# Optimization experiments

Hardware: AMD Instinct MI355X
Metric: run time of the kernel (lower is better)

## Reference

```python
import math
import jax, jax.numpy as jnp
import numpy as np
from jax import lax

B, S, D = 2, 1024, 768
H, E, DH = 12, 8, 64          # n_head, num_experts, head dim
KA = 1                        # top-k experts per head (attention)
KF = 2                        # top-k experts per token (FFN)
DFF = 2048
EMA_DECAY = 0.99
CAP_FACTOR = 1.25
NEG_INF = -1e9


def setup_inputs() -> dict:
    key = jax.random.key(0)
    ks = jax.random.split(key, 16)
    sc = 0.02
    x = jax.random.normal(ks[0], (B, S, D), jnp.float32)
    causal = jnp.tril(jnp.ones((S, S), jnp.float32))
    mask = jnp.where(causal > 0, 0.0, NEG_INF).astype(jnp.float32)
    return {
        "x": x,
        "mask": mask,
        "W_q": jax.random.normal(ks[1], (D, D), jnp.float32) * sc,
        "W_k": jax.random.normal(ks[2], (D, D), jnp.float32) * sc,
        "W_v": jax.random.normal(ks[3], (H, E, DH, DH), jnp.float32) * sc,
        "W_o": jax.random.normal(ks[4], (H, E, DH, DH), jnp.float32) * sc,
        "W_router": jax.random.normal(ks[5], (D, H * E), jnp.float32) * sc,
        "g1": jnp.ones((D,), jnp.float32),
        "b1": jnp.zeros((D,), jnp.float32),
        "g2": jnp.ones((D,), jnp.float32),
        "b2": jnp.zeros((D,), jnp.float32),
        "gate_ff": jax.random.normal(ks[6], (D, E), jnp.float32) * sc,
        "W1": jax.random.normal(ks[7], (E, D, DFF), jnp.float32) * sc,
        "W2": jax.random.normal(ks[8], (E, DFF, D), jnp.float32) * sc,
    }


def layer_norm(x, g, b, eps=1e-5):
    m = jnp.mean(x, -1, keepdims=True)
    v = jnp.var(x, -1, keepdims=True)
    return (x - m) * lax.rsqrt(v + eps) * g + b


def head_switch_attention(x, mask, W_q, W_k, W_v, W_o, W_router):
    b, s, d = x.shape
    q = (x @ W_q).reshape(b, s, H, DH)
    k = (x @ W_k).reshape(b, s, H, DH)
    scores = jnp.einsum("bshd,bthd->bhst", q, k) / math.sqrt(DH) + mask
    p_attn = jax.nn.softmax(scores, axis=-1)          # (B,H,S,S)
    gate_logits = (x @ W_router).reshape(b, s, H, E)
    topk_scores, topk_idx = lax.top_k(gate_logits, KA)  # (B,S,H,KA)
    probs = jax.nn.softmax(topk_scores, axis=-1)
    x_h = x.reshape(b, s, H, DH)
    # value projections for all experts (small d_h x d_h GEMMs)
    v_all = jnp.einsum("bshd,hedf->bshef", x_h, W_v)
    y = jnp.zeros_like(x_h)
    hard_counts = jnp.zeros((H, E), jnp.float32)
    for slot in range(KA):
        oh = jax.nn.one_hot(topk_idx[..., slot], E, dtype=x.dtype)  # (B,S,H,E)
        v_sel = jnp.einsum("bshef,bshe->bshf", v_all, oh)
        # faithful to original einsum 'bhst,hbsd->hbtd' (sums over s)
        attn_out = jnp.einsum("bhst,bshf->bthf", p_attn, v_sel)
        o_all = jnp.einsum("bthf,hefg->btheg", attn_out, W_o)
        o_sel = jnp.einsum("btheg,bthe->bthg", o_all, oh)
        y = y + o_sel * probs[..., slot][..., None]
        hard_counts = hard_counts + lax.stop_gradient(oh).sum((0, 1))
    y = y.reshape(b, s, d)
    # EMA buffers start at zero -> ema = (1-decay)*hard/denom
    ema = hard_counts / (b * s * KA) * (1.0 - EMA_DECAY)
    p_lb = ema / (ema.sum() + 1e-9)
    aux = (p_lb * p_lb).sum() * E * H
    return y, aux


def moe_ffn(x, gate_ff, W1, W2):
    b, s, d = x.shape
    gate_logits = x @ gate_ff                      # (B,S,E), eval: no noise
    topk_scores, topk_idx = lax.top_k(gate_logits, KF)
    probs = jax.nn.softmax(topk_scores, axis=-1)   # (B,S,KF)
    capacity = math.ceil(CAP_FACTOR * (b * s) / E)
    flat_idx = topk_idx.reshape(-1)                # (B*S*KF,)
    oh_flat = jax.nn.one_hot(flat_idx, E, dtype=jnp.float32)
    tokens_so_far = jnp.cumsum(oh_flat, axis=0)
    keep = jnp.take_along_axis(tokens_so_far <= capacity, flat_idx[:, None], axis=1)[:, 0]
    probs = probs * keep.reshape(b, s, KF).astype(probs.dtype)
    probs = probs / (probs.sum(-1, keepdims=True) + 1e-9)
    oh = jax.nn.one_hot(topk_idx, E, dtype=probs.dtype)   # (B,S,KF,E)
    w = (probs[..., None] * oh).sum(2).reshape(b * s, E)  # combined weight per (token, expert)
    xf = x.reshape(b * s, d)
    yf = jnp.zeros_like(xf)
    for e in range(E):
        # scaling applied BEFORE ReLU, matching original x_sel = x * weight
        xe = xf * w[:, e:e + 1]
        yf = yf + jnp.maximum(xe @ W1[e], 0.0) @ W2[e]
    token_ctr = ((probs > 0)[..., None].astype(jnp.float32) * oh).sum((0, 1, 2))
    imp_ctr = (probs[..., None] * oh).sum((0, 1, 2))
    aux = ((token_ctr / token_ctr.sum()) * (imp_ctr / imp_ctr.sum())).sum() * E
    return yf.reshape(b, s, d), aux


def reference(x, mask, W_q, W_k, W_v, W_o, W_router, g1, b1, g2, b2, gate_ff, W1, W2):
    # pre-norm transformer block: x + Attn(LN(x)); x + MoEFFN(LN(x))
    a, aux1 = head_switch_attention(layer_norm(x, g1, b1), mask, W_q, W_k, W_v, W_o, W_router)
    x1 = x + a  # dropout is identity in eval
    f, aux2 = moe_ffn(layer_norm(x1, g2, b2), gate_ff, W1, W2)
    return x1 + f, aux1 + aux2
```

## Files before the change

### kernel.cpp

```cpp
#include <hip/hip_runtime.h>
#include <hip/hip_bf16.h>
#include <cstdint>

typedef __hip_bfloat16 bf16;
typedef __attribute__((ext_vector_type(8))) __bf16 bfrag;
typedef __attribute__((ext_vector_type(4))) float f32x4;

#define B_    2
#define S_    1024
#define D_    768
#define H_    12
#define E_    8
#define DH_   64
#define DFF_  2048
#define CAP_  320
#define CAPP_ 384
#define NTOK  (B_*S_)
#define NTH   (NTOK*H_)
#define QKLD  1536
#define NHE   (H_*E_)

__device__ __forceinline__ void stage16(const bf16* g, bf16* ldsLane){
#if __has_builtin(__builtin_amdgcn_global_load_lds)
  __builtin_amdgcn_global_load_lds((const __attribute__((address_space(1))) unsigned int*)g,
                                   (__attribute__((address_space(3))) unsigned int*)ldsLane, 16, 0, 0);
#else
  *(bfrag*)ldsLane = *(const bfrag*)g;
#endif
}

__global__ __launch_bounds__(256)
void transp_all(const float* __restrict__ Wq, const float* __restrict__ Wk,
                const float* __restrict__ Wr, const float* __restrict__ W1,
                const float* __restrict__ W2,
                bf16* __restrict__ WcatB, float* __restrict__ WrT,
                bf16* __restrict__ WT1, bf16* __restrict__ WT2)
{
  __shared__ float t[64][65];
  int bid = blockIdx.x;
  int tid = threadIdx.x;
  if (bid < 6432){
    const float* src; int N, K, bx, by; bf16* dst;
    if (bid < 144){      src = Wq; N = 768;  K = 768;  bx = bid % 12; by = bid / 12; dst = WcatB; }
    else if (bid < 288){ int r = bid - 144;  src = Wk; N = 768;  K = 768;  bx = r % 12; by = r / 12; dst = WcatB + (long)768*768; }
    else if (bid < 3360){int r = bid - 288;  int e = r / 384; r -= e*384;
                         src = W1 + (long)e*768*2048; N = 2048; K = 768;  bx = r % 32; by = r / 32; dst = WT1 + (long)e*2048*768; }
    else {               int r = bid - 3360; int e = r / 384; r -= e*384;
                         src = W2 + (long)e*2048*768; N = 768;  K = 2048; bx = r % 12; by = r / 12; dst = WT2 + (long)e*768*2048; }
    int n0 = bx*64, k0 = by*64;
    int chunk = tid & 15, rbase = tid >> 4;
#pragma unroll
    for (int rr=0; rr<4; rr++){
      int row = rr*16 + rbase;
      float4 v = *(const float4*)(src + (long)(k0+row)*N + n0 + chunk*4);
      t[row][chunk*4+0] = v.x; t[row][chunk*4+1] = v.y;
      t[row][chunk*4+2] = v.z; t[row][chunk*4+3] = v.w;
    }
    __syncthreads();
#pragma unroll
    for (int rr=0; rr<4; rr++){
      int n = rr*16 + rbase;
      union { ushort4 u; bf16 h[4]; } o;
      o.h[0] = __float2bfloat16(t[chunk*4+0][n]);
      o.h[1] = __float2bfloat16(t[chunk*4+1][n]);
      o.h[2] = __float2bfloat16(t[chunk*4+2][n]);
      o.h[3] = __float2bfloat16(t[chunk*4+3][n]);
      *(ushort4*)(dst + (long)(n0+n)*K + k0 + chunk*4) = o.u;
    }
  } else {
    int r = bid - 6432;
    int n0 = (r % 3)*32, k0 = (r / 3)*64;
    int chunk = tid & 7, row2 = tid >> 3;
#pragma unroll
    for (int rr=0; rr<2; rr++){
      int row = rr*32 + row2;
      float4 v = *(const float4*)(Wr + (long)(k0+row)*96 + n0 + chunk*4);
      t[row][chunk*4+0] = v.x; t[row][chunk*4+1] = v.y;
      t[row][chunk*4+2] = v.z; t[row][chunk*4+3] = v.w;
    }
    __syncthreads();
    int chunkw = tid & 15, nb = tid >> 4;
#pragma unroll
    for (int rr=0; rr<2; rr++){
      int n = rr*16 + nb;
      float4 o;
      o.x = t[chunkw*4+0][n]; o.y = t[chunkw*4+1][n];
      o.z = t[chunkw*4+2][n]; o.w = t[chunkw*4+3][n];
      *(float4*)(WrT + (long)(n0+n)*768 + k0 + chunkw*4) = o;
    }
  }
}

__global__ __launch_bounds__(256)
void gemm_bn64(const bf16* __restrict__ A, const bf16* __restrict__ Bt,
               void* __restrict__ C, void* __restrict__ C2,
               int M, int N, int K, long sA, long sB, long sC, int relu, int outBf, int kSplit)
{
  int nwg = gridDim.x*gridDim.y*gridDim.z;
  int bid = blockIdx.x + gridDim.x*(blockIdx.y + gridDim.y*blockIdx.z);
  int nid = (bid & 7)*(nwg >> 3) + (bid >> 3);
  int bx = nid % gridDim.x;
  int t1 = nid / gridDim.x;
  int by = t1 % gridDim.y;
  int bz = t1 / gridDim.y;
  int e  = bz / kSplit, kc = bz - e*kSplit;
  A  += (long)e*sA;
  Bt += (long)e*sB;
  int kLen = K / kSplit, kBase = kc*kLen;
  int m0 = by*128, n0 = bx*64;
  __shared__ bf16 As[2][128*32];
  __shared__ bf16 Bs[2][64*32];
  int tid = threadIdx.x;
  int w = tid >> 6, lane = tid & 63;
  int quad = lane >> 4, l16 = lane & 15;
  int wm = w*32;
  f32x4 acc[2][4] = {};
  int srow = (lane >> 2);
  int gsw  = ((lane & 3) ^ (srow & 3))*8;
  const bf16* aBase = A + (long)m0*K;
  const bf16* bBase = Bt + (long)n0*K;
  int xr = (l16 & 3);
  int nIt = kLen >> 5;
  {
    int k0 = kBase;
#pragma unroll
    for (int j=0;j<2;j++){
      int c = w*2 + j, row = c*16 + srow;
      stage16(aBase + (long)row*K + k0 + gsw, As[0] + c*512 + lane*8);
    }
    int rowb = w*16 + srow;
    stage16(bBase + (long)rowb*K + k0 + gsw, Bs[0] + w*512 + lane*8);
  }
  int cur = 0;
  for (int it=0; it<nIt; ++it){
    __syncthreads();
    if (it+1 < nIt){
      int k0 = kBase + (it+1)*32;
      int nb = cur^1;
#pragma unroll
      for (int j=0;j<2;j++){
        int c = w*2 + j, row = c*16 + srow;
        stage16(aBase + (long)row*K + k0 + gsw, As[nb] + c*512 + lane*8);
      }
      int rowb = w*16 + srow;
      stage16(bBase + (long)rowb*K + k0 + gsw, Bs[nb] + w*512 + lane*8);
    }
    const bf16* Ac = As[cur];
    const bf16* Bc = Bs[cur];
    bfrag af[2], bfv[4];
#pragma unroll
    for (int t=0;t<2;t++) af[t]  = *(const bfrag*)(Ac + (wm + t*16 + l16)*32 + ((quad ^ xr)*8));
#pragma unroll
    for (int t=0;t<4;t++) bfv[t] = *(const bfrag*)(Bc + (t*16 + l16)*32 + ((quad ^ xr)*8));
#pragma unroll
    for (int ti=0;ti<2;ti++)
#pragma unroll
      for (int tj=0;tj<4;tj++)
        acc[ti][tj] = __builtin_amdgcn_mfma_f32_16x16x32_bf16(af[ti], bfv[tj], acc[ti][tj], 0, 0, 0);
    cur ^= 1;
  }
  long zoff = (long)e*sC;
  void* Cp = kc ? C2 : C;
  if (outBf){
    bf16* Cb = (bf16*)Cp + zoff;
#pragma unroll
    for (int ti=0;ti<2;ti++)
#pragma unroll
      for (int tj=0;tj<4;tj++)
#pragma unroll
        for (int r=0;r<4;r++){
          int row = m0 + wm + ti*16 + quad*4 + r;
          int col = n0 + tj*16 + l16;
          float v = acc[ti][tj][r];
          if (relu) v = fmaxf(v, 0.f);
          Cb[(long)row*N + col] = __float2bfloat16(v);
        }
  } else {
    float* Cf = (float*)Cp + zoff;
#pragma unroll
    for (int ti=0;ti<2;ti++)
#pragma unroll
      for (int tj=0;tj<4;tj++)
#pragma unroll
        for (int r=0;r<4;r++){
          int row = m0 + wm + ti*16 + quad*4 + r;
          int col = n0 + tj*16 + l16;
          float v = acc[ti][tj][r];
          if (relu) v = fmaxf(v, 0.f);
          Cf[(long)row*N + col] = v;
        }
  }
}

__global__ __launch_bounds__(256)
void ln_kernel(const float* __restrict__ src, const float* __restrict__ g, const float* __restrict__ bb,
               float* __restrict__ dstF, bf16* __restrict__ dstB,
               const float* __restrict__ gateW, float* __restrict__ glog2)
{
  int row = blockIdx.x, tid = threadIdx.x;
  __shared__ float red[256];
  __shared__ float gsum[4][E_];
  float v[3];
#pragma unroll
  for (int j=0;j<3;j++) v[j] = src[(long)row*D_ + tid + j*256];
  float s = v[0]+v[1]+v[2];
  red[tid]=s; __syncthreads();
  for (int o=128;o>0;o>>=1){ if(tid<o) red[tid]+=red[tid+o]; __syncthreads(); }
  float mean = red[0]*(1.0f/D_);
  __syncthreads();
  float sq = 0.f;
#pragma unroll
  for (int j=0;j<3;j++){ float d=v[j]-mean; sq += d*d; }
  red[tid]=sq; __syncthreads();
  for (int o=128;o>0;o>>=1){ if(tid<o) red[tid]+=red[tid+o]; __syncthreads(); }
  float rstd = rsqrtf(red[0]*(1.0f/D_) + 1e-5f);
  float ov[3];
#pragma unroll
  for (int j=0;j<3;j++){
    int d = tid + j*256;
    float o = (v[j]-mean)*rstd*g[d] + bb[d];
    ov[j] = o;
    dstF[(long)row*D_+d] = o;
    if (dstB) dstB[(long)row*D_+d] = __float2bfloat16(o);
  }
  if (gateW){
    float gp[E_] = {};
#pragma unroll
    for (int j=0;j<3;j++){
      int d = tid + j*256;
      const float* gw = gateW + (long)d*E_;
#pragma unroll
      for (int e=0;e<E_;e++) gp[e] += ov[j]*gw[e];
    }
#pragma unroll
    for (int off=1; off<64; off<<=1)
#pragma unroll
      for (int e=0;e<E_;e++) gp[e] += __shfl_xor(gp[e], off);
    if ((tid & 63) == 0)
#pragma unroll
      for (int e=0;e<E_;e++) gsum[tid>>6][e] = gp[e];
    __syncthreads();
    if (tid < E_)
      glog2[(long)row*E_ + tid] = gsum[0][tid]+gsum[1][tid]+gsum[2][tid]+gsum[3][tid];
  }
}

#define RTOK 4
__global__ __launch_bounds__(768)
void router_argmax(const float* __restrict__ ln1, const float* __restrict__ WrT,
                   int* __restrict__ eidx, int* __restrict__ gHist,
                   int* __restrict__ hCnt, int* __restrict__ hList)
{
  int tok0 = blockIdx.x*RTOK;
  int tid = threadIdx.x;
  int col = tid >> 3, seg = tid & 7;
  __shared__ float xrow[RTOK][D_];
  __shared__ float logits[RTOK][96];
  for (int i=tid; i<RTOK*D_; i+=768){
    int t = i / D_, dpos = i - t*D_;
    xrow[t][dpos] = ln1[(long)(tok0+t)*D_ + dpos];
  }
  __syncthreads();
  const float* wrow = WrT + (long)col*D_;
  float acc[RTOK] = {};
#pragma unroll
  for (int j=0;j<24;j++){
    int dbase = j*32 + seg*4;
    float4 w = *(const float4*)(wrow + dbase);
#pragma unroll
    for (int t=0;t<RTOK;t++){
      float4 xv = *(const float4*)(&xrow[t][dbase]);
      acc[t] += xv.x*w.x + xv.y*w.y + xv.z*w.z + xv.w*w.w;
    }
  }
#pragma unroll
  for (int off=1; off<8; off<<=1)
#pragma unroll
    for (int t=0;t<RTOK;t++) acc[t] += __shfl_xor(acc[t], off);
  if (seg == 0)
#pragma unroll
    for (int t=0;t<RTOK;t++) logits[t][col] = acc[t];
  __syncthreads();
  if (tid < RTOK*H_){
    int t = tid / H_, h = tid % H_;
    const float* p = &logits[t][h*8];
    float best = p[0]; int bi = 0;
#pragma unroll
    for (int e=1;e<8;e++){ float v=p[e]; if (v > best){ best=v; bi=e; } }
    int tok = tok0 + t;
    eidx[tok*H_ + h] = bi;
    atomicAdd(&gHist[h*E_ + bi], 1);
    int he = h*E_ + bi;
    int pos = atomicAdd(&hCnt[he], 1);
    hList[he*NTOK + pos] = tok;
  }
}

__global__ __launch_bounds__(256)
void vsel_b(const float* __restrict__ ln1, const float* __restrict__ Wv,
            const int* __restrict__ hCnt, const int* __restrict__ hList,
            bf16* __restrict__ vT)
{
  int he = blockIdx.x;
  int h = he >> 3;
  __shared__ float Ws[DH_*DH_];
  __shared__ float xsh[4][DH_];
  int tid = threadIdx.x;
  const float* W = Wv + (long)he*DH_*DH_;
  for (int i=tid; i<DH_*DH_; i+=256) Ws[i] = W[i];
  int cnt = hCnt[he];
  __syncthreads();
  int w = tid >> 6, lane = tid & 63;
  const int* lst = hList + (long)he*NTOK;
  for (int i = blockIdx.y*4 + w; i < cnt; i += 32){
    int tok = lst[i];
    int b = tok >> 10, s = tok & 1023;
    xsh[w][lane] = ln1[(long)tok*D_ + h*DH_ + lane];
    float acc = 0.f;
#pragma unroll 8
    for (int d=0; d<DH_; d++) acc += xsh[w][d]*Ws[d*DH_ + lane];
    vT[((long)(b*H_+h)*DH_ + lane)*S_ + s] = __float2bfloat16(acc);
  }
}

__global__ __launch_bounds__(256)
void attn_stats_mfma(const bf16* __restrict__ qkB, float* __restrict__ gM, float* __restrict__ gL)
{
  int h = blockIdx.y, b = blockIdx.z;
  int tid = threadIdx.x;
  int w = tid >> 6, lane = tid & 63;
  int quad = lane >> 4, l16 = lane & 15;
  int x7 = l16 & 7;
  __shared__ bf16 ldsQ[64*64];
  __shared__ bf16 ldsK[2][64*64];
  const bf16* kbase = qkB + ((long)(b*S_))*QKLD + 768 + h*DH_;
  for (int half=0; half<2; half++){
    int s0 = (half ? (S_/64 - 1 - blockIdx.x) : blockIdx.x)*64;
    __syncthreads();
    const bf16* qbase = qkB + ((long)(b*S_ + s0))*QKLD + h*DH_;
#pragma unroll
    for (int j=0;j<2;j++){
      int c = j*256 + tid;
      int row = c >> 3;
      int gs = ((c & 7) ^ (row & 7))*8;
      stage16(qbase + (long)row*QKLD + gs, ldsQ + c*8);
      stage16(kbase + (long)row*QKLD + gs, ldsK[0] + c*8);
    }
    float m_ln[4] = {-1e30f,-1e30f,-1e30f,-1e30f};
    float l_ln[4] = {0.f,0.f,0.f,0.f};
    int ttEnd = s0 >> 6;
    int cur = 0;
    for (int tt=0; tt<=ttEnd; tt++){
      __syncthreads();
      if (tt < ttEnd){
#pragma unroll
        for (int j=0;j<2;j++){
          int c = j*256 + tid;
          int row = c >> 3;
          int gs = ((c & 7) ^ (row & 7))*8;
          stage16(kbase + (long)((tt+1)*64 + row)*QKLD + gs, ldsK[cur^1] + c*8);
        }
      }
      const bf16* Kc = ldsK[cur];
      bfrag af0 = *(const bfrag*)(ldsQ + (w*16 + l16)*64 + ((quad     ^ x7)*8));
      bfrag af1 = *(const bfrag*)(ldsQ + (w*16 + l16)*64 + (((quad+4) ^ x7)*8));
      f32x4 cfr[4];
#pragma unroll
      for (int j=0;j<4;j++){
        bfrag b0 = *(const bfrag*)(Kc + (j*16 + l16)*64 + ((quad     ^ x7)*8));
        bfrag b1 = *(const bfrag*)(Kc + (j*16 + l16)*64 + (((quad+4) ^ x7)*8));
        f32x4 z = {};
        z = __builtin_amdgcn_mfma_f32_16x16x32_bf16(af0, b0, z, 0,0,0);
        z = __builtin_amdgcn_mfma_f32_16x16x32_bf16(af1, b1, z, 0,0,0);
        cfr[j] = z;
      }
#pragma unroll
      for (int r=0;r<4;r++){
        int s_g = s0 + w*16 + quad*4 + r;
        float v0 = (tt*64      + l16 <= s_g) ? cfr[0][r]*0.125f : -1e30f;
        float v1 = (tt*64 + 16 + l16 <= s_g) ? cfr[1][r]*0.125f : -1e30f;
        float v2 = (tt*64 + 32 + l16 <= s_g) ? cfr[2][r]*0.125f : -1e30f;
        float v3 = (tt*64 + 48 + l16 <= s_g) ? cfr[3][r]*0.125f : -1e30f;
        float mt = fmaxf(fmaxf(v0,v1), fmaxf(v2,v3));
        float mn = fmaxf(m_ln[r], mt);
        l_ln[r] = l_ln[r]*__expf(m_ln[r]-mn)
                + ((__expf(v0-mn)+__expf(v1-mn)) + (__expf(v2-mn)+__expf(v3-mn)));
        m_ln[r] = mn;
      }
      cur ^= 1;
    }
#pragma unroll
    for (int r=0;r<4;r++){
      float mf = m_ln[r];
#pragma unroll
      for (int mm=1; mm<16; mm<<=1) mf = fmaxf(mf, __shfl_xor(mf, mm));
      float lf = l_ln[r]*__expf(m_ln[r]-mf);
#pragma unroll
      for (int mm=1; mm<16; mm<<=1) lf += __shfl_xor(lf, mm);
      if (l16 == 0){
        long basei = ((long)(b*H_ + h))*S_ + s0 + w*16 + quad*4 + r;
        gM[basei] = mf; gL[basei] = lf;
      }
    }
  }
}

__global__ __launch_bounds__(256)
void attn_pv(const bf16* __restrict__ qkB, const bf16* __restrict__ vT,
             const float* __restrict__ gM, const float* __restrict__ gL, float* __restrict__ aoH)
{
  int h = blockIdx.y, b = blockIdx.z;
  int bh = b*H_ + h;
  int tid = threadIdx.x;
  int w = tid >> 6, lane = tid & 63;
  int quad = lane >> 4, l16 = lane & 15;
  int x7 = l16 & 7;
  __shared__ bf16 ldsK[64*64];
  __shared__ bf16 ldsQ[2][64*64];
  __shared__ bf16 ldsV[2][64*64];
  __shared__ bf16 ldsS[64*72];
  __shared__ float smx[2][64], sli[2][64];
  const bf16* qbase = qkB + ((long)(b*S_))*QKLD + h*DH_;
  const bf16* vbase = vT + ((long)bh*DH_)*S_;
  for (int half=0; half<2; half++){
    int t0 = (half ? (S_/64 - 1 - blockIdx.x) : blockIdx.x)*64;
    __syncthreads();
    const bf16* kbase = qkB + ((long)(b*S_ + t0))*QKLD + 768 + h*DH_;
    int sb0 = t0 >> 6;
#pragma unroll
    for (int j=0;j<2;j++){
      int c = j*256 + tid;
      int row = c >> 3;
      int gs = ((c & 7) ^ (row & 7))*8;
      stage16(kbase + (long)row*QKLD + gs, ldsK + c*8);
      stage16(qbase + (long)(sb0*64 + row)*QKLD + gs, ldsQ[0] + c*8);
      stage16(vbase + (long)row*S_ + sb0*64 + gs, ldsV[0] + c*8);
    }
    if (tid < 64){
      smx[0][tid] = gM[(long)bh*S_ + sb0*64 + tid];
      sli[0][tid] = 1.0f / gL[(long)bh*S_ + sb0*64 + tid];
    }
    f32x4 accO[4] = {};
    int cur = 0;
    for (int sb = sb0; sb < S_/64; sb++){
      __syncthreads();
      if (sb+1 < S_/64){
        int nb = cur^1;
#pragma unroll
        for (int j=0;j<2;j++){
          int c = j*256 + tid;
          int row = c >> 3;
          int gs = ((c & 7) ^ (row & 7))*8;
          stage16(qbase + (long)((sb+1)*64 + row)*QKLD + gs, ldsQ[nb] + c*8);
          stage16(vbase + (long)row*S_ + (sb+1)*64 + gs, ldsV[nb] + c*8);
        }
        if (tid < 64){
          smx[nb][tid] = gM[(long)bh*S_ + (sb+1)*64 + tid];
          sli[nb][tid] = 1.0f / gL[(long)bh*S_ + (sb+1)*64 + tid];
        }
      }
      const bf16* Qc = ldsQ[cur];
      const bf16* Vc = ldsV[cur];
      bfrag af0 = *(const bfrag*)(ldsK + (w*16 + l16)*64 + ((quad     ^ x7)*8));
      bfrag af1 = *(const bfrag*)(ldsK + (w*16 + l16)*64 + (((quad+4) ^ x7)*8));
      f32x4 cs[4];
#pragma unroll
      for (int j=0;j<4;j++){
        bfrag b0 = *(const bfrag*)(Qc + (j*16 + l16)*64 + ((quad     ^ x7)*8));
        bfrag b1 = *(const bfrag*)(Qc + (j*16 + l16)*64 + (((quad+4) ^ x7)*8));
        f32x4 z = {};
        z = __builtin_amdgcn_mfma_f32_16x16x32_bf16(af0, b0, z, 0,0,0);
        z = __builtin_amdgcn_mfma_f32_16x16x32_bf16(af1, b1, z, 0,0,0);
        cs[j] = z;
      }
#pragma unroll
      for (int j=0;j<4;j++)
#pragma unroll
        for (int r=0;r<4;r++){
          int t_loc = w*16 + quad*4 + r;
          int s_loc = j*16 + l16;
          float wgt = ((t0 + t_loc) <= (sb*64 + s_loc))
                    ? __expf(cs[j][r]*0.125f - smx[cur][s_loc])*sli[cur][s_loc] : 0.f;
          ldsS[t_loc*72 + s_loc] = __float2bfloat16(wgt);
        }
      bfrag pa0 = *(const bfrag*)(ldsS + (w*16 + l16)*72 + quad*8);
      bfrag pa1 = *(const bfrag*)(ldsS + (w*16 + l16)*72 + 32 + quad*8);
#pragma unroll
      for (int j=0;j<4;j++){
        bfrag b0 = *(const bfrag*)(Vc + (j*16 + l16)*64 + ((quad     ^ x7)*8));
        bfrag b1 = *(const bfrag*)(Vc + (j*16 + l16)*64 + (((quad+4) ^ x7)*8));
        accO[j] = __builtin_amdgcn_mfma_f32_16x16x32_bf16(pa0, b0, accO[j], 0,0,0);
        accO[j] = __builtin_amdgcn_mfma_f32_16x16x32_bf16(pa1, b1, accO[j], 0,0,0);
      }
      cur ^= 1;
    }
#pragma unroll
    for (int j=0;j<4;j++)
#pragma unroll
      for (int r=0;r<4;r++){
        int t_loc = w*16 + quad*4 + r;
        int f = j*16 + l16;
        aoH[((long)bh*S_ + t0 + t_loc)*DH_ + f] = accO[j][r];
      }
  }
}

__global__ __launch_bounds__(256)
void oproj_b(const float* __restrict__ aoH, const float* __restrict__ Wo,
             const int* __restrict__ hCnt, const int* __restrict__ hList,
             const float* __restrict__ x, float* __restrict__ x1)
{
  int he = blockIdx.x;
  int h = he >> 3;
  __shared__ float Ws[DH_*DH_];
  __shared__ float xsh[4][DH_];
  int tid = threadIdx.x;
  const float* W = Wo + (long)he*DH_*DH_;
  for (int i=tid; i<DH_*DH_; i+=256) Ws[i] = W[i];
  int cnt = hCnt[he];
  __syncthreads();
  int w = tid >> 6, lane = tid & 63;
  const int* lst = hList + (long)he*NTOK;
  for (int i = blockIdx.y*4 + w; i < cnt; i += 32){
    int tok = lst[i];
    int b = tok >> 10, s = tok & 1023;
    xsh[w][lane] = aoH[((long)(b*H_+h)*S_ + s)*DH_ + lane];
    float acc = 0.f;
#pragma unroll 8
    for (int f=0; f<DH_; f++) acc += xsh[w][f]*Ws[f*DH_ + lane];
    long idx = (long)tok*D_ + h*DH_ + lane;
    x1[idx] = x[idx] + acc;
  }
}

__global__ __launch_bounds__(256)
void route_kernel(const float* __restrict__ glog2, const int* __restrict__ gHist,
                  int* __restrict__ gI0, int* __restrict__ gI1,
                  int* __restrict__ gPos0, int* __restrict__ gPos1,
                  int* __restrict__ listTok, float* __restrict__ listW,
                  int* __restrict__ gCnt, float* __restrict__ auxOut)
{
  __shared__ unsigned char sI0[NTOK], sI1[NTOK];
  __shared__ float sP0[NTOK], sP1[NTOK];
  __shared__ short sPos0[NTOK], sPos1[NTOK];
  __shared__ int   sScan[256*E_];
  __shared__ int   sHist[H_*E_];
  __shared__ float sImp[E_];
  __shared__ int   sCnt[E_];
  int tid = threadIdx.x;
  if (tid < E_) sImp[tid] = 0.f;
  if (tid < H_*E_) sHist[tid] = gHist[tid];
  for (int i=tid; i<NTOK; i+=256){
    const float* p = glog2 + (long)i*E_;
    float b0 = p[0]; int e0 = 0;
#pragma unroll
    for (int e=1;e<E_;e++){ float vv=p[e]; if (vv > b0){ b0=vv; e0=e; } }
    float b1v = -1e30f; int e1 = 0;
#pragma unroll
    for (int e=0;e<E_;e++){ if (e==e0) continue; float vv=p[e]; if (vv > b1v){ b1v=vv; e1=e; } }
    float ex = __expf(b1v - b0);
    float inv = 1.f/(1.f + ex);
    sI0[i] = (unsigned char)e0; sI1[i] = (unsigned char)e1;
    sP0[i] = inv; sP1[i] = ex*inv;
    gI0[i] = e0; gI1[i] = e1;
  }
  __syncthreads();
  {
    int myCnt[E_] = {};
#pragma unroll
    for (int j=0;j<16;j++){
      int i = tid*16 + j;
      int tok = i >> 1;
      int e = (i & 1) ? (int)sI1[tok] : (int)sI0[tok];
      myCnt[e]++;
    }
#pragma unroll
    for (int e=0;e<E_;e++) sScan[tid*E_+e] = myCnt[e];
    __syncthreads();
    for (int off=1; off<256; off<<=1){
      int v[E_];
      if (tid >= off){
#pragma unroll
        for (int e=0;e<E_;e++) v[e] = sScan[(tid-off)*E_+e];
      }
      __syncthreads();
      if (tid >= off){
#pragma unroll
        for (int e=0;e<E_;e++) sScan[tid*E_+e] += v[e];
      }
      __syncthreads();
    }
    int pref[E_];
#pragma unroll
    for (int e=0;e<E_;e++) pref[e] = tid ? sScan[(tid-1)*E_+e] : 0;
#pragma unroll
    for (int j=0;j<16;j++){
      int i = tid*16 + j;
      int tok = i >> 1;
      int e = (i & 1) ? (int)sI1[tok] : (int)sI0[tok];
      int pos = pref[e]++;
      short p = (pos < CAP_) ? (short)pos : (short)-1;
      if (i & 1) sPos1[tok] = p; else sPos0[tok] = p;
    }
    if (tid < E_){
      int cnt = sScan[255*E_ + tid];
      sCnt[tid] = cnt < CAP_ ? cnt : CAP_;
      gCnt[tid] = sCnt[tid];
    }
  }
  __syncthreads();
  for (int i=tid; i<NTOK; i+=256){
    int e0 = sI0[i], e1 = sI1[i];
    int p0i = sPos0[i], p1i = sPos1[i];
    float k0 = p0i >= 0 ? 1.f : 0.f, k1 = p1i >= 0 ? 1.f : 0.f;
    float p0 = sP0[i], p1 = sP1[i];
    float denom = p0*k0 + p1*k1 + 1e-9f;
    float w0 = p0*k0/denom, w1 = p1*k1/denom;
    if (p0i >= 0){ listTok[e0*CAP_+p0i] = i; listW[e0*CAP_+p0i] = w0; atomicAdd(&sImp[e0], w0); }
    if (p1i >= 0){ listTok[e1*CAP_+p1i] = i; listW[e1*CAP_+p1i] = w1; atomicAdd(&sImp[e1], w1); }
    gPos0[i] = p0i; gPos1[i] = p1i;
  }
  __syncthreads();
  if (tid == 0){
    float tot = 0.f;
    for (int i=0;i<H_*E_;i++) tot += (float)sHist[i]*(1.0f/NTOK)*0.01f;
    float a1 = 0.f;
    for (int i=0;i<H_*E_;i++){
      float p = ((float)sHist[i]*(1.0f/NTOK)*0.01f)/(tot + 1e-9f);
      a1 += p*p;
    }
    a1 *= (float)(H_*E_);
    float tcs = 0.f, ims = 0.f;
    for (int e=0;e<E_;e++){ tcs += (float)sCnt[e]; ims += sImp[e]; }
    float a2 = 0.f;
    for (int e=0;e<E_;e++) a2 += ((float)sCnt[e]/tcs)*(sImp[e]/ims);
    a2 *= (float)E_;
    auxOut[0] = a1 + a2;
  }
}

__global__ __launch_bounds__(256)
void gather_kernel(const float* __restrict__ ln2, const int* __restrict__ listTok,
                   const float* __restrict__ listW, const int* __restrict__ gCnt,
                   bf16* __restrict__ Xg)
{
  int blk = blockIdx.x;
  int e = blk / CAPP_, r = blk % CAPP_;
  int tid = threadIdx.x;
  bool live = r < gCnt[e];
  int tok = 0; float w = 0.f;
  if (live){ tok = listTok[e*CAP_+r]; w = listW[e*CAP_+r]; }
  for (int d=tid; d<D_; d+=256)
    Xg[(long)blk*D_ + d] = __float2bfloat16(live ? ln2[(long)tok*D_+d]*w : 0.f);
}

__global__ __launch_bounds__(256)
void combine_kernel(const float* __restrict__ x1,
                    const float* __restrict__ Ya, const float* __restrict__ Yb,
                    const int* __restrict__ gI0, const int* __restrict__ gI1,
                    const int* __restrict__ gPos0, const int* __restrict__ gPos1,
                    float* __restrict__ out)
{
  int i = blockIdx.x;
  int tid = threadIdx.x;
  int p0 = gPos0[i], p1 = gPos1[i];
  int e0 = gI0[i],  e1 = gI1[i];
  long off0 = (long)(e0*CAPP_ + (p0 >= 0 ? p0 : 0))*D_;
  long off1 = (long)(e1*CAPP_ + (p1 >= 0 ? p1 : 0))*D_;
  const float* y0a = Ya + off0; const float* y0b = Yb + off0;
  const float* y1a = Ya + off1; const float* y1b = Yb + off1;
  for (int d=tid; d<D_; d+=256){
    float v = x1[(long)i*D_+d];
    if (p0 >= 0) v += y0a[d] + y0b[d];
    if (p1 >= 0) v += y1a[d] + y1b[d];
    out[(long)i*D_+d] = v;
  }
}

extern "C" void kernel_launch(void* const* d_in, const int* in_sizes, int n_in,
                              void* d_out, int out_size, void* d_ws, size_t ws_size,
                              hipStream_t stream)
{
  const float* x    = (const float*)d_in[0];
  const float* W_q  = (const float*)d_in[2];
  const float* W_k  = (const float*)d_in[3];
  const float* W_v  = (const float*)d_in[4];
  const float* W_o  = (const float*)d_in[5];
  const float* W_r  = (const float*)d_in[6];
  const float* g1   = (const float*)d_in[7];
  const float* b1   = (const float*)d_in[8];
  const float* g2   = (const float*)d_in[9];
  const float* b2   = (const float*)d_in[10];
  const float* gate = (const float*)d_in[11];
  const float* W1   = (const float*)d_in[12];
  const float* W2   = (const float*)d_in[13];
  float* out = (float*)d_out;

  float* wsf = (float*)d_ws;
  const long oX1   = 0;
  const long oLnF  = 1572864;
  const long oLnB  = 3145728;
  const long oWcat = 3932160;
  const long oWrT  = 4521984;
  const long oHist = 4595712;
  const long oHCnt = 4595808;
  const long oGM   = 4718592;
  const long oGL   = 4743168;
  const long oEidx = 4767744;
  const long oGlg2 = 4792320;
  const long oI0   = 4808704;
  const long oI1   = 4810752;
  const long oP0   = 4812800;
  const long oP1   = 4814848;
  const long oLT   = 4816896;
  const long oLW   = 4819456;
  const long oCnt  = 4822016;
  const long SB    = 4822528;
  const long oWT1  = SB + 12976128;
  const long oWT2  = oWT1 + 6291456;
  const long TOTAL = oWT2 + 6291456;
  if (ws_size < (size_t)TOTAL*4) return;

  float* x1    = wsf + oX1;
  float* lnbF  = wsf + oLnF;
  bf16*  lnbB  = (bf16*)(wsf + oLnB);
  bf16*  WcatB = (bf16*)(wsf + oWcat);
  float* WrT   = wsf + oWrT;
  int*   gHist = (int*)(wsf + oHist);
  int*   hCnt  = (int*)(wsf + oHCnt);
  float* gM    = wsf + oGM;
  float* gL    = wsf + oGL;
  int*   eidx  = (int*)(wsf + oEidx);
  float* glog2 = wsf + oGlg2;
  int*   gI0   = (int*)(wsf + oI0);
  int*   gI1   = (int*)(wsf + oI1);
  int*   gPos0 = (int*)(wsf + oP0);
  int*   gPos1 = (int*)(wsf + oP1);
  int*   lTok  = (int*)(wsf + oLT);
  float* lW    = wsf + oLW;
  int*   gCnt  = (int*)(wsf + oCnt);
  bf16*  qkB   = (bf16*)(wsf + SB);
  bf16*  vT    = (bf16*)(wsf + SB + 1572864);
  float* aoH   = wsf + SB + 2359296;
  int*   hList = (int*)(wsf + SB + 3932160);
  bf16*  Xg    = (bf16*)(wsf + SB + 6291456);
  bf16*  Hid   = (bf16*)(wsf + SB + 7471104);
  float* Yexp  = wsf + SB + 10616832;
  float* YexpB = wsf + oLnF;
  bf16*  WT1   = (bf16*)(wsf + oWT1);
  bf16*  WT2   = (bf16*)(wsf + oWT2);

  hipMemsetAsync(gHist, 0, 2*NHE*sizeof(int), stream);
  transp_all<<<6468,256,0,stream>>>(W_q, W_k, W_r, W1, W2, WcatB, WrT, WT1, WT2);

  ln_kernel<<<NTOK,256,0,stream>>>(x, g1, b1, lnbF, lnbB, nullptr, nullptr);
  gemm_bn64<<<dim3(24,16,1),256,0,stream>>>(lnbB, WcatB, qkB, nullptr, 2048, QKLD, 768, 0,0,0, 0, 1, 1);
  router_argmax<<<NTOK/RTOK,768,0,stream>>>(lnbF, WrT, eidx, gHist, hCnt, hList);
  vsel_b<<<dim3(NHE,8,1),256,0,stream>>>(lnbF, W_v, hCnt, hList, vT);
  attn_stats_mfma<<<dim3(S_/128,H_,B_),256,0,stream>>>(qkB, gM, gL);
  attn_pv<<<dim3(S_/128,H_,B_),256,0,stream>>>(qkB, vT, gM, gL, aoH);
  oproj_b<<<dim3(NHE,8,1),256,0,stream>>>(aoH, W_o, hCnt, hList, x, x1);

  ln_kernel<<<NTOK,256,0,stream>>>(x1, g2, b2, lnbF, nullptr, gate, glog2);
  route_kernel<<<1,256,0,stream>>>(glog2, gHist, gI0,gI1,gPos0,gPos1, lTok,lW,gCnt, out + (size_t)NTOK*D_);
  gather_kernel<<<E_*CAPP_,256,0,stream>>>(lnbF, lTok, lW, gCnt, Xg);
  gemm_bn64<<<dim3(32,3,8),256,0,stream>>>(Xg, WT1, Hid, nullptr, CAPP_, DFF_, 768,
                                           (long)CAPP_*768, (long)2048*768, (long)CAPP_*2048, 1, 1, 1);
  gemm_bn64<<<dim3(12,3,16),256,0,stream>>>(Hid, WT2, Yexp, YexpB, CAPP_, 768, 2048,
                                            (long)CAPP_*2048, (long)768*2048, (long)CAPP_*768, 0, 0, 2);
  combine_kernel<<<NTOK,256,0,stream>>>(x1, Yexp, YexpB, gI0,gI1,gPos0,gPos1, out);
}
```

Baseline: 394.8 us.

## Fuse token gather and weighting into FFN1 GEMM; widen weight transpose tiles

Removes the separate gather kernel by having a new FFN1 GEMM load routed token rows from the fp32 layernorm output, scale them by the routing weight and convert to bf16 while staging the A tile, with register double-buffering. The weight transpose kernel now handles 128-row tiles per block, uses a swizzled LDS layout with float4 stores and writes 16-byte bf16 vectors, halving the block count. This cuts a kernel launch and the Xg round trip through memory, at the cost of fp32 scattered A loads inside the GEMM loop.

```diff
diff --git a/kernel.cpp b/kernel.cpp
--- a/kernel.cpp
+++ b/kernel.cpp
@@ -36,53 +36,52 @@
                 bf16* __restrict__ WcatB, float* __restrict__ WrT,
                 bf16* __restrict__ WT1, bf16* __restrict__ WT2)
 {
-  __shared__ float t[64][65];
-  int bid = blockIdx.x;
-  int tid = threadIdx.x;
-  if (bid < 6432){
+  __shared__ float t[128][64];
+  int bid = blockIdx.x, tid = threadIdx.x;
+  if (bid < 3216){
     const float* src; int N, K, bx, by; bf16* dst;
-    if (bid < 144){      src = Wq; N = 768;  K = 768;  bx = bid % 12; by = bid / 12; dst = WcatB; }
-    else if (bid < 288){ int r = bid - 144;  src = Wk; N = 768;  K = 768;  bx = r % 12; by = r / 12; dst = WcatB + (long)768*768; }
-    else if (bid < 3360){int r = bid - 288;  int e = r / 384; r -= e*384;
-                         src = W1 + (long)e*768*2048; N = 2048; K = 768;  bx = r % 32; by = r / 32; dst = WT1 + (long)e*2048*768; }
-    else {               int r = bid - 3360; int e = r / 384; r -= e*384;
-                         src = W2 + (long)e*2048*768; N = 768;  K = 2048; bx = r % 12; by = r / 12; dst = WT2 + (long)e*768*2048; }
-    int n0 = bx*64, k0 = by*64;
-    int chunk = tid & 15, rbase = tid >> 4;
-#pragma unroll
-    for (int rr=0; rr<4; rr++){
-      int row = rr*16 + rbase;
+    if (bid < 72)      {                src = Wq; N=768;  K=768;  bx=bid%12; by=bid/12; dst=WcatB; }
+    else if (bid <144) { int r=bid-72;  src = Wk; N=768;  K=768;  bx=r%12;   by=r/12;   dst=WcatB+(long)768*768; }
+    else if (bid<1680) { int r=bid-144; int e=r/192; r-=e*192;
+                         src = W1+(long)e*768*2048; N=2048; K=768;  bx=r%32; by=r/32;   dst=WT1+(long)e*2048*768; }
+    else               { int r=bid-1680; int e=r/192; r-=e*192;
+                         src = W2+(long)e*2048*768; N=768;  K=2048; bx=r%12; by=r/12;   dst=WT2+(long)e*768*2048; }
+    int n0 = bx*64, k0 = by*128;
+    int chunk = tid & 15, rgrp = tid >> 4;
+#pragma unroll
+    for (int rr=0; rr<8; rr++){
+      int row = rr*16 + rgrp;
       float4 v = *(const float4*)(src + (long)(k0+row)*N + n0 + chunk*4);
-      t[row][chunk*4+0] = v.x; t[row][chunk*4+1] = v.y;
-      t[row][chunk*4+2] = v.z; t[row][chunk*4+3] = v.w;
+      *(float4*)&t[row][((chunk ^ (row>>3)) & 15)*4] = v;
     }
     __syncthreads();
 #pragma unroll
-    for (int rr=0; rr<4; rr++){
-      int n = rr*16 + rbase;
-      union { ushort4 u; bf16 h[4]; } o;
-      o.h[0] = __float2bfloat16(t[chunk*4+0][n]);
-      o.h[1] = __float2bfloat16(t[chunk*4+1][n]);
-      o.h[2] = __float2bfloat16(t[chunk*4+2][n]);
-      o.h[3] = __float2bfloat16(t[chunk*4+3][n]);
-      *(ushort4*)(dst + (long)(n0+n)*K + k0 + chunk*4) = o.u;
+    for (int it=0; it<4; it++){
+      int slot = it*256 + tid;
+      int n = slot >> 4, kc = slot & 15;
+      union { bfrag f; bf16 h[8]; } o;
+#pragma unroll
+      for (int i=0;i<8;i++){
+        int row = kc*8 + i;
+        o.h[i] = __float2bfloat16(t[row][n ^ (kc*4)]);
+      }
+      *(bfrag*)(dst + (long)(n0+n)*K + k0 + kc*8) = o.f;
     }
   } else {
-    int r = bid - 6432;
+    int r = bid - 3216;
     int n0 = (r % 3)*32, k0 = (r / 3)*64;
     int chunk = tid & 7, row2 = tid >> 3;
 #pragma unroll
     for (int rr=0; rr<2; rr++){
       int row = rr*32 + row2;
       float4 v = *(const float4*)(Wr + (long)(k0+row)*96 + n0 + chunk*4);
-      t[row][chunk*4+0] = v.x; t[row][chunk*4+1] = v.y;
-      t[row][chunk*4+2] = v.z; t[row][chunk*4+3] = v.w;
+      *(float4*)&t[row][chunk*4] = v;
     }
     __syncthreads();
-    int chunkw = tid & 15, nb = tid >> 4;
+    int chunkw = tid & 15, ng = tid >> 4;
 #pragma unroll
     for (int rr=0; rr<2; rr++){
-      int n = rr*16 + nb;
+      int n = rr*16 + ng;
       float4 o;
       o.x = t[chunkw*4+0][n]; o.y = t[chunkw*4+1][n];
       o.z = t[chunkw*4+2][n]; o.w = t[chunkw*4+3][n];
@@ -193,6 +192,109 @@
 }
 
 __global__ __launch_bounds__(256)
+void gemm_ffn1(const float* __restrict__ ln2, const bf16* __restrict__ Bt, bf16* __restrict__ C,
+               const int* __restrict__ lTok, const float* __restrict__ lW, const int* __restrict__ gCnt)
+{
+  int nwg = gridDim.x*gridDim.y*gridDim.z;
+  int bid = blockIdx.x + gridDim.x*(blockIdx.y + gridDim.y*blockIdx.z);
+  int nid = (bid & 7)*(nwg >> 3) + (bid >> 3);
+  int bx = nid % gridDim.x;
+  int t1 = nid / gridDim.x;
+  int by = t1 % gridDim.y;
+  int e  = t1 / gridDim.y;
+  int m0 = by*128;
+  const bf16* bBase = Bt + (long)e*2048*768 + (long)(bx*64)*768;
+  __shared__ bf16 As[2][128*32];
+  __shared__ bf16 Bs[2][64*32];
+  int tid = threadIdx.x;
+  int w = tid >> 6, lane = tid & 63;
+  int quad = lane >> 4, l16 = lane & 15;
+  int wm = w*32;
+  f32x4 acc[2][4] = {};
+  int srow = (lane >> 2);
+  int gsw  = ((lane & 3) ^ (srow & 3))*8;
+  int xr = (l16 & 3);
+  int cnt = gCnt[e];
+  int tokA[2]; float wA[2];
+#pragma unroll
+  for (int j=0;j<2;j++){
+    int row = m0 + (w*2+j)*16 + srow;
+    bool live = row < cnt;
+    tokA[j] = live ? lTok[e*CAP_ + row] : 0;
+    wA[j]   = live ? lW[e*CAP_ + row]   : 0.f;
+  }
+  const int nIt = 24;
+  {
+#pragma unroll
+    for (int j=0;j<2;j++){
+      const float* src = ln2 + (long)tokA[j]*D_ + gsw;
+      float4 a0 = *(const float4*)(src);
+      float4 a1 = *(const float4*)(src+4);
+      union { bfrag f; bf16 h[8]; } o;
+      o.h[0]=__float2bfloat16(a0.x*wA[j]); o.h[1]=__float2bfloat16(a0.y*wA[j]);
+      o.h[2]=__float2bfloat16(a0.z*wA[j]); o.h[3]=__float2bfloat16(a0.w*wA[j]);
+      o.h[4]=__float2bfloat16(a1.x*wA[j]); o.h[5]=__float2bfloat16(a1.y*wA[j]);
+      o.h[6]=__float2bfloat16(a1.z*wA[j]); o.h[7]=__float2bfloat16(a1.w*wA[j]);
+      *(bfrag*)(As[0] + (w*2+j)*512 + lane*8) = o.f;
+    }
+    int rowb = w*16 + srow;
+    stage16(bBase + (long)rowb*768 + gsw, Bs[0] + w*512 + lane*8);
+  }
+  int cur = 0;
+  for (int it=0; it<nIt; ++it){
+    __syncthreads();
+    float4 a0[2], a1[2];
+    if (it+1 < nIt){
+      int k0 = (it+1)*32;
+#pragma unroll
+      for (int j=0;j<2;j++){
+        const float* src = ln2 + (long)tokA[j]*D_ + k0 + gsw;
+        a0[j] = *(const float4*)(src);
+        a1[j] = *(const float4*)(src+4);
+      }
+      int rowb = w*16 + srow;
+      stage16(bBase + (long)rowb*768 + k0 + gsw, Bs[cur^1] + w*512 + lane*8);
+    }
+    const bf16* Ac = As[cur];
+    const bf16* Bc = Bs[cur];
+    bfrag af[2], bfv[4];
+#pragma unroll
+    for (int t=0;t<2;t++) af[t]  = *(const bfrag*)(Ac + (wm + t*16 + l16)*32 + ((quad ^ xr)*8));
+#pragma unroll
+    for (int t=0;t<4;t++) bfv[t] = *(const bfrag*)(Bc + (t*16 + l16)*32 + ((quad ^ xr)*8));
+#pragma unroll
+    for (int ti=0;ti<2;ti++)
+#pragma unroll
+      for (int tj=0;tj<4;tj++)
+        acc[ti][tj] = __builtin_amdgcn_mfma_f32_16x16x32_bf16(af[ti], bfv[tj], acc[ti][tj], 0, 0, 0);
+    if (it+1 < nIt){
+      int nb = cur^1;
+#pragma unroll
+      for (int j=0;j<2;j++){
+        union { bfrag f; bf16 h[8]; } o;
+        o.h[0]=__float2bfloat16(a0[j].x*wA[j]); o.h[1]=__float2bfloat16(a0[j].y*wA[j]);
+        o.h[2]=__float2bfloat16(a0[j].z*wA[j]); o.h[3]=__float2bfloat16(a0[j].w*wA[j]);
+        o.h[4]=__float2bfloat16(a1[j].x*wA[j]); o.h[5]=__float2bfloat16(a1[j].y*wA[j]);
+        o.h[6]=__float2bfloat16(a1[j].z*wA[j]); o.h[7]=__float2bfloat16(a1[j].w*wA[j]);
+        *(bfrag*)(As[nb] + (w*2+j)*512 + lane*8) = o.f;
+      }
+    }
+    cur ^= 1;
+  }
+  bf16* Cb = C + (long)e*CAPP_*DFF_;
+#pragma unroll
+  for (int ti=0;ti<2;ti++)
+#pragma unroll
+    for (int tj=0;tj<4;tj++)
+#pragma unroll
+      for (int r=0;r<4;r++){
+        int row = m0 + wm + ti*16 + quad*4 + r;
+        int col = bx*64 + tj*16 + l16;
+        Cb[(long)row*DFF_ + col] = __float2bfloat16(fmaxf(acc[ti][tj][r], 0.f));
+      }
+}
+
+__global__ __launch_bounds__(256)
 void ln_kernel(const float* __restrict__ src, const float* __restrict__ g, const float* __restrict__ bb,
                float* __restrict__ dstF, bf16* __restrict__ dstB,
                const float* __restrict__ gateW, float* __restrict__ glog2)
@@ -637,21 +739,6 @@
     a2 *= (float)E_;
     auxOut[0] = a1 + a2;
   }
-}
-
-__global__ __launch_bounds__(256)
-void gather_kernel(const float* __restrict__ ln2, const int* __restrict__ listTok,
-                   const float* __restrict__ listW, const int* __restrict__ gCnt,
-                   bf16* __restrict__ Xg)
-{
-  int blk = blockIdx.x;
-  int e = blk / CAPP_, r = blk % CAPP_;
-  int tid = threadIdx.x;
-  bool live = r < gCnt[e];
-  int tok = 0; float w = 0.f;
-  if (live){ tok = listTok[e*CAP_+r]; w = listW[e*CAP_+r]; }
-  for (int d=tid; d<D_; d+=256)
-    Xg[(long)blk*D_ + d] = __float2bfloat16(live ? ln2[(long)tok*D_+d]*w : 0.f);
 }
 
 __global__ __launch_bounds__(256)
@@ -743,7 +830,6 @@
   bf16*  vT    = (bf16*)(wsf + SB + 1572864);
   float* aoH   = wsf + SB + 2359296;
   int*   hList = (int*)(wsf + SB + 3932160);
-  bf16*  Xg    = (bf16*)(wsf + SB + 6291456);
   bf16*  Hid   = (bf16*)(wsf + SB + 7471104);
   float* Yexp  = wsf + SB + 10616832;
   float* YexpB = wsf + oLnF;
@@ -751,7 +837,7 @@
   bf16*  WT2   = (bf16*)(wsf + oWT2);
 
   hipMemsetAsync(gHist, 0, 2*NHE*sizeof(int), stream);
-  transp_all<<<6468,256,0,stream>>>(W_q, W_k, W_r, W1, W2, WcatB, WrT, WT1, WT2);
+  transp_all<<<3252,256,0,stream>>>(W_q, W_k, W_r, W1, W2, WcatB, WrT, WT1, WT2);
 
   ln_kernel<<<NTOK,256,0,stream>>>(x, g1, b1, lnbF, lnbB, nullptr, nullptr);
   gemm_bn64<<<dim3(24,16,1),256,0,stream>>>(lnbB, WcatB, qkB, nullptr, 2048, QKLD, 768, 0,0,0, 0, 1, 1);
@@ -763,9 +849,7 @@
 
   ln_kernel<<<NTOK,256,0,stream>>>(x1, g2, b2, lnbF, nullptr, gate, glog2);
   route_kernel<<<1,256,0,stream>>>(glog2, gHist, gI0,gI1,gPos0,gPos1, lTok,lW,gCnt, out + (size_t)NTOK*D_);
-  gather_kernel<<<E_*CAPP_,256,0,stream>>>(lnbF, lTok, lW, gCnt, Xg);
-  gemm_bn64<<<dim3(32,3,8),256,0,stream>>>(Xg, WT1, Hid, nullptr, CAPP_, DFF_, 768,
-                                           (long)CAPP_*768, (long)2048*768, (long)CAPP_*2048, 1, 1, 1);
+  gemm_ffn1<<<dim3(32,3,8),256,0,stream>>>(lnbF, WT1, Hid, lTok, lW, gCnt);
   gemm_bn64<<<dim3(12,3,16),256,0,stream>>>(Hid, WT2, Yexp, YexpB, CAPP_, 768, 2048,
                                             (long)CAPP_*2048, (long)768*2048, (long)CAPP_*768, 0, 0, 2);
   combine_kernel<<<NTOK,256,0,stream>>>(x1, Yexp, YexpB, gI0,gI1,gPos0,gPos1, out);
```

After: 395.6 us. About the same (+0.2%).
